# Performance work log

Measured on AMD Instinct MI355X. Metric: run time of the kernel, lower is better.

## Reference

```python
import jax, jax.numpy as jnp
import numpy as np

H = 8          # num_heads
SCALE = 25.0   # attention temperature
THRESH = 0.75  # raw cosine-similarity mask threshold


def _l2n(x):
    return x / jnp.linalg.norm(x, axis=-1, keepdims=True)


def setup_inputs() -> dict:
    key = jax.random.key(0)
    ks = jax.random.split(key, 8)
    B, N, C, OUT = 1, 2048, 1024, 1024
    s = 0.02
    return {
        "x_cls": jax.random.normal(ks[0], (B, N, C), jnp.float32),
        "x_reg": jax.random.normal(ks[1], (B, N, C), jnp.float32),
        "cls_score": jax.random.uniform(ks[2], (N,), jnp.float32),
        "fg_score": jax.random.uniform(ks[3], (N,), jnp.float32),
        "W_qkv_cls": jax.random.normal(ks[4], (3 * C, C), jnp.float32) * s,
        "W_qkv_reg": jax.random.normal(ks[5], (3 * C, C), jnp.float32) * s,
        "W1": jax.random.normal(ks[6], (2 * C, 2 * C), jnp.float32) * s,
        "b1": jnp.zeros((2 * C,), jnp.float32),
        "W2": jax.random.normal(ks[7], (OUT, 4 * C), jnp.float32) * s,
        "b2": jnp.zeros((OUT,), jnp.float32),
    }


def reference(x_cls, x_reg, cls_score, fg_score, W_qkv_cls, W_qkv_reg, W1, b1, W2, b2):
    B, N, C = x_cls.shape
    d = C // H

    def split_qkv(x, W):
        # nn.Linear (no bias): x @ W.T, then [B,N,3,H,d] -> [3,B,H,N,d]
        qkv = (x @ W.T).reshape(B, N, 3, H, d).transpose(2, 0, 3, 1, 4)
        return qkv[0], qkv[1], qkv[2]

    q_cls, k_cls, v_cls = split_qkv(x_cls, W_qkv_cls)
    q_reg, k_reg, _ = split_qkv(x_reg, W_qkv_reg)

    q_cls, k_cls = _l2n(q_cls), _l2n(k_cls)
    q_reg, k_reg = _l2n(q_reg), _l2n(k_reg)
    v_cls_n = _l2n(v_cls)

    cs = cls_score.reshape(1, 1, 1, N)  # broadcast over [B,H,N,N]
    fs = fg_score.reshape(1, 1, 1, N)

    attn_cls_raw = jnp.einsum('bhnd,bhmd->bhnm', v_cls_n, v_cls_n)
    attn_cls = jax.nn.softmax(jnp.einsum('bhnd,bhmd->bhnm', q_cls, k_cls) * SCALE * cs, axis=-1)
    attn_reg = jax.nn.softmax(jnp.einsum('bhnd,bhmd->bhnm', q_reg, k_reg) * SCALE * fs, axis=-1)
    attn = (attn_reg + attn_cls) * 0.5

    x = jnp.einsum('bhnm,bhmd->bhnd', attn, v_cls).transpose(0, 2, 1, 3).reshape(B, N, C)
    x_ori = v_cls.transpose(0, 2, 1, 3).reshape(B, N, C)
    trans_cls = jnp.concatenate([x, x_ori], axis=-1)  # [B,N,2C]

    # head-averaged similarity, masked and re-normalized (batch element 0)
    sim_raw = attn_cls_raw.sum(axis=1)[0] / H          # [N,N]
    sim_mask = (sim_raw > THRESH).astype(x_cls.dtype)
    sim_attn = attn.sum(axis=1)[0] / H
    sim_round2 = jax.nn.softmax(sim_attn, axis=-1)
    masked = sim_mask * sim_round2
    sim_round2 = masked / masked.sum(axis=-1, keepdims=True)

    msa = trans_cls @ W1.T + b1                        # linear1 [B,N,2C]
    feat = msa[0]                                      # [N,2C]
    soft_sim = sim_round2 @ feat                       # [N,2C]
    ave = jnp.concatenate([soft_sim, feat], axis=-1)   # [N,4C]
    out = ave @ W2.T + b2                              # [N,OUT]
    return out
```

## Files before the change

### kernel.cpp

```cpp
#include <hip/hip_runtime.h>
#include <math.h>

#define PN 2048
#define PC 1024
#define PH 8
#define PD 128
#define PC3 3072

typedef __bf16 bf16x8 __attribute__((ext_vector_type(8)));
typedef float  f32x4  __attribute__((ext_vector_type(4)));
typedef short  s8v    __attribute__((ext_vector_type(8)));
typedef short  s4v    __attribute__((ext_vector_type(4)));

__device__ __forceinline__ short f2bf(float x) {
    unsigned u = __float_as_uint(x);
    unsigned r = (u + 0x7fffu + ((u >> 16) & 1u)) >> 16;
    return (short)r;
}
__device__ __forceinline__ float bf2f(short s) {
    return __uint_as_float(((unsigned)(unsigned short)s) << 16);
}

#define LDS_DMA(g, l) __builtin_amdgcn_global_load_lds( \
    (const __attribute__((address_space(1))) void*)(g), \
    (__attribute__((address_space(3))) void*)(l), 16, 0, 0)

__device__ __forceinline__ void stage128(const short* g, long ld, short* lds,
                                         int wave, int lrow, int lcol)
{
#pragma unroll
    for (int kc = 0; kc < 4; ++kc) {
        LDS_DMA(g + (long)lrow * ld + kc * 32 + lcol, lds + kc * 4096 + wave * 512);
        LDS_DMA(g + (long)(lrow + 64) * ld + kc * 32 + lcol,
                lds + kc * 4096 + 2048 + wave * 512);
    }
}

template<int BN, bool OBF16, bool BIAS>
__global__ __launch_bounds__(256) void mfma_gemm_k(
    const short* __restrict__ A, int lda, long zsa,
    const short* __restrict__ B, int ldb, long zsb,
    void* __restrict__ Cv, int ldc, long zsc,
    int K, float alpha, const float* __restrict__ bias)
{
    constexpr int NJ = BN / 32;
    __shared__ short As[128 * 32];
    __shared__ short Bs[BN * 32];
    const int tid = threadIdx.x;
    const int wave = tid >> 6, lane = tid & 63;
    const int lrow = tid >> 2;
    const int lcol = (tid & 3) * 8;
    const int z = blockIdx.z;
    A += (long)z * zsa;
    B += (long)z * zsb;
    const int row0 = blockIdx.y * 128, col0 = blockIdx.x * BN;
    const short* Ag = A + (long)(row0 + lrow) * lda + lcol;
    const short* Bg = B + (long)(col0 + lrow) * ldb + lcol;
    short* AsW0 = As + wave * 512;
    short* AsW1 = As + 2048 + wave * 512;
    short* BsW0 = Bs + wave * 512;
    short* BsW1 = Bs + 2048 + wave * 512;
    const int wr = (wave >> 1) * 64, wc = (wave & 1) * (BN / 2);
    const int m16 = lane & 15, q8 = (lane >> 4) * 8;

    f32x4 acc[4][NJ];
#pragma unroll
    for (int i = 0; i < 4; ++i)
#pragma unroll
        for (int j = 0; j < NJ; ++j) acc[i][j] = (f32x4){0.f, 0.f, 0.f, 0.f};

    for (int kt = 0; kt < K; kt += 32) {
        if (kt) __syncthreads();
        LDS_DMA(Ag + kt, AsW0);
        LDS_DMA(Ag + kt + 64 * (long)lda, AsW1);
        LDS_DMA(Bg + kt, BsW0);
        if (BN == 128) LDS_DMA(Bg + kt + 64 * (long)ldb, BsW1);
        __syncthreads();
        bf16x8 a[4], b[NJ];
#pragma unroll
        for (int i = 0; i < 4; ++i)
            a[i] = *(const bf16x8*)&As[(wr + i * 16 + m16) * 32 + q8];
#pragma unroll
        for (int j = 0; j < NJ; ++j)
            b[j] = *(const bf16x8*)&Bs[(wc + j * 16 + m16) * 32 + q8];
#pragma unroll
        for (int i = 0; i < 4; ++i)
#pragma unroll
            for (int j = 0; j < NJ; ++j)
                acc[i][j] = __builtin_amdgcn_mfma_f32_16x16x32_bf16(a[i], b[j], acc[i][j], 0, 0, 0);
    }

    const long cz = (long)z * zsc;
#pragma unroll
    for (int i = 0; i < 4; ++i) {
        const int r0 = row0 + wr + i * 16 + (lane >> 4) * 4;
#pragma unroll
        for (int j = 0; j < NJ; ++j) {
            const int c = col0 + wc + j * 16 + m16;
            const float bv = BIAS ? bias[c] : 0.0f;
#pragma unroll
            for (int t = 0; t < 4; ++t) {
                const float x = acc[i][j][t] * alpha + bv;
                const long off = cz + (long)(r0 + t) * ldc + c;
                if (OBF16) ((short*)Cv)[off] = f2bf(x);
                else       ((float*)Cv)[off] = x;
            }
        }
    }
}

__global__ __launch_bounds__(256) void attn_rowsum_k(
    const short* __restrict__ qkv,
    const float* __restrict__ cls_score, const float* __restrict__ fg_score,
    float* __restrict__ l_g)
{
    __shared__ short Qs[16384];
    __shared__ short Ks[2][16384];
    __shared__ float lsum[128][2];
    const int tid = threadIdx.x, wave = tid >> 6, lane = tid & 63;
    const int lrow = tid >> 2, lcol = (tid & 3) * 8;
    const int wr = (wave >> 1) * 64, wc = (wave & 1) * 64;
    const int m16 = lane & 15, q4 = lane >> 4, q8 = q4 * 8;
    const int row0 = blockIdx.x * 128, h = blockIdx.y, side = blockIdx.z;
    const float* sc_g = side ? fg_score : cls_score;
    const short* base = qkv + (long)side * PN * PC3 + h * PD;
    const short* Kg = base + PC;
    stage128(base + (long)row0 * PC3, PC3, Qs, wave, lrow, lcol);
    stage128(Kg, PC3, Ks[0], wave, lrow, lcol);
    bf16x8 a[4][4];
    float rs[4][4] = {};
    for (int ct = 0; ct < 16; ++ct) {
        __syncthreads();
        if (ct == 0) {
#pragma unroll
            for (int i = 0; i < 4; ++i)
#pragma unroll
                for (int kc = 0; kc < 4; ++kc)
                    a[i][kc] = *(const bf16x8*)&Qs[kc * 4096 + (wr + i * 16 + m16) * 32 + q8];
        }
        if (ct < 15)
            stage128(Kg + (long)(ct + 1) * 128 * PC3, PC3, Ks[(ct + 1) & 1], wave, lrow, lcol);
        const short* kb = Ks[ct & 1];
        f32x4 acc[4][4];
#pragma unroll
        for (int i = 0; i < 4; ++i)
#pragma unroll
            for (int j = 0; j < 4; ++j) acc[i][j] = (f32x4){0.f, 0.f, 0.f, 0.f};
#pragma unroll
        for (int kc = 0; kc < 4; ++kc) {
            bf16x8 b[4];
#pragma unroll
            for (int j = 0; j < 4; ++j)
                b[j] = *(const bf16x8*)&kb[kc * 4096 + (wc + j * 16 + m16) * 32 + q8];
#pragma unroll
            for (int i = 0; i < 4; ++i)
#pragma unroll
                for (int j = 0; j < 4; ++j)
                    acc[i][j] = __builtin_amdgcn_mfma_f32_16x16x32_bf16(a[i][kc], b[j], acc[i][j], 0, 0, 0);
        }
#pragma unroll
        for (int j = 0; j < 4; ++j) {
            const float s25 = 25.0f * sc_g[ct * 128 + wc + j * 16 + m16];
#pragma unroll
            for (int i = 0; i < 4; ++i)
#pragma unroll
                for (int t = 0; t < 4; ++t)
                    rs[i][t] += __expf(acc[i][j][t] * s25);
        }
    }
#pragma unroll
    for (int i = 0; i < 4; ++i)
#pragma unroll
        for (int t = 0; t < 4; ++t) {
            float v = rs[i][t];
            v += __shfl_xor(v, 1, 64); v += __shfl_xor(v, 2, 64);
            v += __shfl_xor(v, 4, 64); v += __shfl_xor(v, 8, 64);
            if (m16 == 0) lsum[wr + i * 16 + q4 * 4 + t][wave & 1] = v;
        }
    __syncthreads();
    if (tid < 128)
        l_g[((long)side * PH + h) * PN + row0 + tid] = lsum[tid][0] + lsum[tid][1];
}

__global__ __launch_bounds__(256) void attn_combine_k(
    const short* __restrict__ qkv,
    const float* __restrict__ cls_score, const float* __restrict__ fg_score,
    const float* __restrict__ l_g,
    short* __restrict__ attn8, float* __restrict__ sim_attn)
{
    __shared__ short Ts[65536];
    const int tid = threadIdx.x, wave = tid >> 6, lane = tid & 63;
    const int lrow = tid >> 2, lcol = (tid & 3) * 8;
    const int wr = (wave >> 1) * 64, wc = (wave & 1) * 64;
    const int m16 = lane & 15, q4 = lane >> 4, q8 = q4 * 8;
    const int col0 = blockIdx.x * 128, row0 = blockIdx.y * 128;
    const long NN = (long)PN * PN;

    {
        const short* b0 = qkv;
        stage128(b0 + (long)row0 * PC3, PC3, Ts, wave, lrow, lcol);
        stage128(b0 + PC + (long)col0 * PC3, PC3, Ts + 16384, wave, lrow, lcol);
    }

    f32x4 sim[4][4];
#pragma unroll
    for (int i = 0; i < 4; ++i)
#pragma unroll
        for (int j = 0; j < 4; ++j) sim[i][j] = (f32x4){0.f, 0.f, 0.f, 0.f};
    f32x4 comb[4][4];

    for (int st = 0; st < 16; ++st) {
        const int h = st >> 1, s = st & 1;
        __syncthreads();
        if (st < 15) {
            const int h2 = (st + 1) >> 1, s2 = (st + 1) & 1;
            const short* b2 = qkv + (long)s2 * PN * PC3 + h2 * PD;
            short* dst = Ts + ((st + 1) & 1) * 32768;
            stage128(b2 + (long)row0 * PC3, PC3, dst, wave, lrow, lcol);
            stage128(b2 + PC + (long)col0 * PC3, PC3, dst + 16384, wave, lrow, lcol);
        }
        const short* Qb = Ts + (st & 1) * 32768;
        const short* Kb = Qb + 16384;

        float rl[4][4];
#pragma unroll
        for (int i = 0; i < 4; ++i)
#pragma unroll
            for (int t = 0; t < 4; ++t)
                rl[i][t] = 0.5f / l_g[((long)s * PH + h) * PN + row0 + wr + i * 16 + q4 * 4 + t];

        f32x4 acc[4][4];
#pragma unroll
        for (int i = 0; i < 4; ++i)
#pragma unroll
            for (int j = 0; j < 4; ++j) acc[i][j] = (f32x4){0.f, 0.f, 0.f, 0.f};
#pragma unroll
        for (int kc = 0; kc < 4; ++kc) {
            bf16x8 a[4], b[4];
#pragma unroll
            for (int i = 0; i < 4; ++i)
                a[i] = *(const bf16x8*)&Qb[kc * 4096 + (wr + i * 16 + m16) * 32 + q8];
#pragma unroll
            for (int j = 0; j < 4; ++j)
                b[j] = *(const bf16x8*)&Kb[kc * 4096 + (wc + j * 16 + m16) * 32 + q8];
#pragma unroll
            for (int i = 0; i < 4; ++i)
#pragma unroll
                for (int j = 0; j < 4; ++j)
                    acc[i][j] = __builtin_amdgcn_mfma_f32_16x16x32_bf16(a[i], b[j], acc[i][j], 0, 0, 0);
        }
        const float* sc_g = s ? fg_score : cls_score;
#pragma unroll
        for (int j = 0; j < 4; ++j) {
            const float s25 = 25.0f * sc_g[col0 + wc + j * 16 + m16];
#pragma unroll
            for (int i = 0; i < 4; ++i)
#pragma unroll
                for (int t = 0; t < 4; ++t) {
                    const float e = __expf(acc[i][j][t] * s25) * rl[i][t];
                    comb[i][j][t] = s ? (comb[i][j][t] + e) : e;
                }
        }
        if (s) {
#pragma unroll
            for (int i = 0; i < 4; ++i)
#pragma unroll
                for (int t = 0; t < 4; ++t) {
                    const long rbase = (long)h * NN +
                        (long)(row0 + wr + i * 16 + q4 * 4 + t) * PN + col0 + wc + m16;
#pragma unroll
                    for (int j = 0; j < 4; ++j)
                        attn8[rbase + j * 16] = f2bf(comb[i][j][t]);
                }
#pragma unroll
            for (int i = 0; i < 4; ++i)
#pragma unroll
                for (int j = 0; j < 4; ++j)
#pragma unroll
                    for (int t = 0; t < 4; ++t)
                        sim[i][j][t] += comb[i][j][t] * 0.125f;
        }
    }
#pragma unroll
    for (int i = 0; i < 4; ++i)
#pragma unroll
        for (int t = 0; t < 4; ++t) {
            const long rbase = (long)(row0 + wr + i * 16 + q4 * 4 + t) * PN + col0 + wc + m16;
#pragma unroll
            for (int j = 0; j < 4; ++j)
                sim_attn[rbase + j * 16] = sim[i][j][t];
        }
}

__global__ __launch_bounds__(256) void f2bf_k(const float* __restrict__ src,
                                              short* __restrict__ dst, int n4)
{
    const int i = blockIdx.x * 256 + threadIdx.x;
    if (i < n4) {
        float4 v = ((const float4*)src)[i];
        s4v o;
        o[0] = f2bf(v.x); o[1] = f2bf(v.y); o[2] = f2bf(v.z); o[3] = f2bf(v.w);
        ((s4v*)dst)[i] = o;
    }
}

__global__ __launch_bounds__(256) void transpose_bf16_k(
    const short* __restrict__ src, int sld, short* __restrict__ dst, int dld)
{
    __shared__ short tl[64][72];
    const int r0 = blockIdx.y * 64, c0 = blockIdx.x * 64;
    const int tr = threadIdx.x >> 2;
    const int tc = (threadIdx.x & 3) * 16;
    const short* sp = src + (long)(r0 + tr) * sld + c0 + tc;
    s8v v0 = *(const s8v*)sp;
    s8v v1 = *(const s8v*)(sp + 8);
    *(s8v*)&tl[tr][tc] = v0;
    *(s8v*)&tl[tr][tc + 8] = v1;
    __syncthreads();
    s8v o0, o1;
#pragma unroll
    for (int k = 0; k < 8; ++k) { o0[k] = tl[tc + k][tr]; o1[k] = tl[tc + 8 + k][tr]; }
    short* dp = dst + (long)(c0 + tr) * dld + r0 + tc;
    *(s8v*)dp = o0;
    *(s8v*)(dp + 8) = o1;
}

__global__ __launch_bounds__(256) void norm_qk_k(short* __restrict__ qkv)
{
    short* p = qkv + (long)blockIdx.z * ((long)PN * PC3)
                   + (long)blockIdx.x * PC3 + blockIdx.y * PC + threadIdx.x * 4;
    s4v v = *(s4v*)p;
    float f0 = bf2f(v[0]), f1 = bf2f(v[1]), f2 = bf2f(v[2]), f3 = bf2f(v[3]);
    float ss = f0 * f0 + f1 * f1 + f2 * f2 + f3 * f3;
    ss += __shfl_xor(ss, 16, 64); ss += __shfl_xor(ss, 8, 64);
    ss += __shfl_xor(ss, 4, 64);  ss += __shfl_xor(ss, 2, 64);
    ss += __shfl_xor(ss, 1, 64);
    const float rn = rsqrtf(ss);
    s4v o;
    o[0] = f2bf(f0 * rn); o[1] = f2bf(f1 * rn); o[2] = f2bf(f2 * rn); o[3] = f2bf(f3 * rn);
    *(s4v*)p = o;
}

__global__ __launch_bounds__(256) void norm_v_k(const short* __restrict__ qkv_cls,
                                                short* __restrict__ Vn,
                                                short* __restrict__ trans)
{
    const int n = blockIdx.x, t = threadIdx.x;
    const short* p = qkv_cls + (long)n * PC3 + 2 * PC + t * 4;
    s4v v = *(const s4v*)p;
    float f0 = bf2f(v[0]), f1 = bf2f(v[1]), f2 = bf2f(v[2]), f3 = bf2f(v[3]);
    float ss = f0 * f0 + f1 * f1 + f2 * f2 + f3 * f3;
    ss += __shfl_xor(ss, 16, 64); ss += __shfl_xor(ss, 8, 64);
    ss += __shfl_xor(ss, 4, 64);  ss += __shfl_xor(ss, 2, 64);
    ss += __shfl_xor(ss, 1, 64);
    const float rn = rsqrtf(ss);
    s4v o;
    o[0] = f2bf(f0 * rn); o[1] = f2bf(f1 * rn); o[2] = f2bf(f2 * rn); o[3] = f2bf(f3 * rn);
    *(s4v*)(Vn + (long)n * PC + t * 4) = o;
    *(s4v*)(trans + (long)n * (2 * PC) + PC + t * 4) = v;
}

__device__ __forceinline__ float wave_sum(float v) {
#pragma unroll
    for (int o = 32; o > 0; o >>= 1) v += __shfl_xor(v, o, 64);
    return v;
}
__device__ __forceinline__ float wave_max(float v) {
#pragma unroll
    for (int o = 32; o > 0; o >>= 1) v = fmaxf(v, __shfl_xor(v, o, 64));
    return v;
}
__device__ __forceinline__ float block_sum(float v, float* sm) {
    v = wave_sum(v);
    __syncthreads();
    if ((threadIdx.x & 63) == 0) sm[threadIdx.x >> 6] = v;
    __syncthreads();
    return sm[0] + sm[1] + sm[2] + sm[3];
}
__device__ __forceinline__ float block_max(float v, float* sm) {
    v = wave_max(v);
    __syncthreads();
    if ((threadIdx.x & 63) == 0) sm[threadIdx.x >> 6] = v;
    __syncthreads();
    return fmaxf(fmaxf(sm[0], sm[1]), fmaxf(sm[2], sm[3]));
}

__global__ __launch_bounds__(256) void sim_round2_k(
    const float* __restrict__ S, const short* __restrict__ Sraw,
    short* __restrict__ Sout)
{
    __shared__ float sm[4];
    const long row = (long)blockIdx.x * PN;
    const int t = threadIdx.x;
    float v[8];
    bool keep[8];
#pragma unroll
    for (int j = 0; j < 8; ++j) {
        const int m = t + 256 * j;
        v[j] = S[row + m];
        keep[j] = bf2f(Sraw[row + m]) > 0.75f;
    }
    float mx = -1e30f;
#pragma unroll
    for (int j = 0; j < 8; ++j) mx = fmaxf(mx, v[j]);
    mx = block_max(mx, sm);
    float sum = 0.f;
#pragma unroll
    for (int j = 0; j < 8; ++j) { v[j] = __expf(v[j] - mx); sum += v[j]; }
    sum = block_sum(sum, sm);
    const float inv = 1.0f / sum;
    float msum = 0.f;
#pragma unroll
    for (int j = 0; j < 8; ++j) { v[j] = keep[j] ? v[j] * inv : 0.f; msum += v[j]; }
    msum = block_sum(msum, sm);
    const float minv = 1.0f / msum;
#pragma unroll
    for (int j = 0; j < 8; ++j) {
        const int m = t + 256 * j;
        Sout[row + m] = f2bf(v[j] * minv);
    }
}

extern "C" void kernel_launch(void* const* d_in, const int* in_sizes, int n_in,
                              void* d_out, int out_size, void* d_ws, size_t ws_size,
                              hipStream_t stream)
{
    (void)in_sizes; (void)n_in; (void)out_size; (void)ws_size;
    const float* x_cls = (const float*)d_in[0];
    const float* x_reg = (const float*)d_in[1];
    const float* cls_score = (const float*)d_in[2];
    const float* fg_score = (const float*)d_in[3];
    const float* Wqc = (const float*)d_in[4];
    const float* Wqr = (const float*)d_in[5];
    const float* W1 = (const float*)d_in[6];
    const float* b1 = (const float*)d_in[7];
    const float* W2 = (const float*)d_in[8];
    const float* b2 = (const float*)d_in[9];
    float* out = (float*)d_out;

    char* w = (char*)d_ws;
    short* qkv_cls_bf = (short*)(w + ((size_t)0   << 20));
    short* qkv_reg_bf = (short*)(w + ((size_t)12  << 20));
    short* attn8      = (short*)(w + ((size_t)24  << 20));
    float* sim_attn   = (float*)(w + ((size_t)88  << 20));
    short* sim_raw_bf = (short*)(w + ((size_t)104 << 20));
    short* Vn         = (short*)(w + ((size_t)112 << 20));
    short* vT         = (short*)(w + ((size_t)116 << 20));
    short* W1_bf      = (short*)(w + ((size_t)120 << 20));
    short* W2_bf      = (short*)(w + ((size_t)128 << 20));
    short* x_cls_bf   = (short*)(w + ((size_t)136 << 20));
    short* x_reg_bf   = (short*)(w + ((size_t)140 << 20));
    short* Wqc_bf     = (short*)(w + ((size_t)144 << 20));
    short* Wqr_bf     = (short*)(w + ((size_t)150 << 20));
    float* l_g        = (float*)(w + ((size_t)160 << 20));
    short* trans      = (short*)(w + ((size_t)136 << 20));
    short* ave        = (short*)(w + ((size_t)144 << 20));
    short* sim_bf     = (short*)(w + ((size_t)24  << 20));
    short* featT      = (short*)(w + ((size_t)32  << 20));

    const long NN = (long)PN * PN;

    f2bf_k<<<2048, 256, 0, stream>>>(x_cls, x_cls_bf, PN * PC / 4);
    f2bf_k<<<2048, 256, 0, stream>>>(x_reg, x_reg_bf, PN * PC / 4);
    f2bf_k<<<3072, 256, 0, stream>>>(Wqc, Wqc_bf, PC3 * PC / 4);
    f2bf_k<<<3072, 256, 0, stream>>>(Wqr, Wqr_bf, PC3 * PC / 4);
    f2bf_k<<<4096, 256, 0, stream>>>(W1, W1_bf, 2 * PC * 2 * PC / 4);
    f2bf_k<<<4096, 256, 0, stream>>>(W2, W2_bf, PC * 4 * PC / 4);

    mfma_gemm_k<128, true, false><<<dim3(24, 16, 1), 256, 0, stream>>>(
        x_cls_bf, PC, 0, Wqc_bf, PC, 0, qkv_cls_bf, PC3, 0, PC, 1.0f, nullptr);
    mfma_gemm_k<128, true, false><<<dim3(16, 16, 1), 256, 0, stream>>>(
        x_reg_bf, PC, 0, Wqr_bf, PC, 0, qkv_reg_bf, PC3, 0, PC, 1.0f, nullptr);

    norm_qk_k<<<dim3(PN, 2, 2), 256, 0, stream>>>(qkv_cls_bf);
    norm_v_k<<<dim3(PN), 256, 0, stream>>>(qkv_cls_bf, Vn, trans);
    transpose_bf16_k<<<dim3(PC / 64, PN / 64), 256, 0, stream>>>(
        qkv_cls_bf + 2 * PC, PC3, vT, PN);

    mfma_gemm_k<128, true, false><<<dim3(16, 16, 1), 256, 0, stream>>>(
        Vn, PC, 0, Vn, PC, 0, sim_raw_bf, PN, 0, PC, 0.125f, nullptr);

    attn_rowsum_k<<<dim3(16, PH, 2), 256, 0, stream>>>(
        qkv_cls_bf, cls_score, fg_score, l_g);
    attn_combine_k<<<dim3(16, 16), 256, 0, stream>>>(
        qkv_cls_bf, cls_score, fg_score, l_g, attn8, sim_attn);

    mfma_gemm_k<64, true, false><<<dim3(2, 16, PH), 256, 0, stream>>>(
        attn8, PN, NN, vT, PN, (long)PD * PN, trans, 2 * PC, PD, PN, 1.0f, nullptr);

    sim_round2_k<<<PN, 256, 0, stream>>>(sim_attn, sim_raw_bf, sim_bf);

    mfma_gemm_k<128, true, true><<<dim3(16, 16, 1), 256, 0, stream>>>(
        trans, 2 * PC, 0, W1_bf, 2 * PC, 0, ave + 2 * PC, 4 * PC, 0, 2 * PC, 1.0f, b1);

    transpose_bf16_k<<<dim3(32, 32), 256, 0, stream>>>(ave + 2 * PC, 4 * PC, featT, 2 * PC);

    mfma_gemm_k<128, true, false><<<dim3(16, 16, 1), 256, 0, stream>>>(
        sim_bf, 2 * PC, 0, featT, 2 * PC, 0, ave, 4 * PC, 0, 2 * PC, 1.0f, nullptr);

    mfma_gemm_k<64, false, true><<<dim3(16, 16, 1), 256, 0, stream>>>(
        ave, 4 * PC, 0, W2_bf, 4 * PC, 0, out, PC, 0, 4 * PC, 1.0f, b2);
}
```

Measured before the change: 507.3 us.

## Single-buffer attention LDS, vectorize combine stores, merge conversion and norm launches

The attention rowsum and combine kernels drop LDS double buffering for a single buffer with extra barriers, halving shared memory per block so more blocks can be resident per CU. The combine kernel swaps the MFMA operand order so each lane holds contiguous columns, which lets it issue 4-wide vector stores for attn8 and sim_attn. The six fp32-to-bf16 conversion launches are merged into one kernel over a contiguous workspace, and the QK and V normalisation kernels are merged into one launch. The trade-off is that global loads no longer overlap with MFMA work inside a block, so the change relies on higher occupancy to hide that latency.

```diff
diff --git a/kernel.cpp b/kernel.cpp
--- a/kernel.cpp
+++ b/kernel.cpp
@@ -115,7 +115,7 @@
     float* __restrict__ l_g)
 {
     __shared__ short Qs[16384];
-    __shared__ short Ks[2][16384];
+    __shared__ short Ks[16384];
     __shared__ float lsum[128][2];
     const int tid = threadIdx.x, wave = tid >> 6, lane = tid & 63;
     const int lrow = tid >> 2, lcol = (tid & 3) * 8;
@@ -126,21 +126,21 @@
     const short* base = qkv + (long)side * PN * PC3 + h * PD;
     const short* Kg = base + PC;
     stage128(base + (long)row0 * PC3, PC3, Qs, wave, lrow, lcol);
-    stage128(Kg, PC3, Ks[0], wave, lrow, lcol);
+    stage128(Kg, PC3, Ks, wave, lrow, lcol);
+    __syncthreads();
     bf16x8 a[4][4];
+#pragma unroll
+    for (int i = 0; i < 4; ++i)
+#pragma unroll
+        for (int kc = 0; kc < 4; ++kc)
+            a[i][kc] = *(const bf16x8*)&Qs[kc * 4096 + (wr + i * 16 + m16) * 32 + q8];
     float rs[4][4] = {};
     for (int ct = 0; ct < 16; ++ct) {
-        __syncthreads();
-        if (ct == 0) {
-#pragma unroll
-            for (int i = 0; i < 4; ++i)
-#pragma unroll
-                for (int kc = 0; kc < 4; ++kc)
-                    a[i][kc] = *(const bf16x8*)&Qs[kc * 4096 + (wr + i * 16 + m16) * 32 + q8];
-        }
-        if (ct < 15)
-            stage128(Kg + (long)(ct + 1) * 128 * PC3, PC3, Ks[(ct + 1) & 1], wave, lrow, lcol);
-        const short* kb = Ks[ct & 1];
+        if (ct) {
+            __syncthreads();
+            stage128(Kg + (long)ct * 128 * PC3, PC3, Ks, wave, lrow, lcol);
+            __syncthreads();
+        }
         f32x4 acc[4][4];
 #pragma unroll
         for (int i = 0; i < 4; ++i)
@@ -151,7 +151,7 @@
             bf16x8 b[4];
 #pragma unroll
             for (int j = 0; j < 4; ++j)
-                b[j] = *(const bf16x8*)&kb[kc * 4096 + (wc + j * 16 + m16) * 32 + q8];
+                b[j] = *(const bf16x8*)&Ks[kc * 4096 + (wc + j * 16 + m16) * 32 + q8];
 #pragma unroll
             for (int i = 0; i < 4; ++i)
 #pragma unroll
@@ -188,7 +188,7 @@
     const float* __restrict__ l_g,
     short* __restrict__ attn8, float* __restrict__ sim_attn)
 {
-    __shared__ short Ts[65536];
+    __shared__ short Ts[32768];
     const int tid = threadIdx.x, wave = tid >> 6, lane = tid & 63;
     const int lrow = tid >> 2, lcol = (tid & 3) * 8;
     const int wr = (wave >> 1) * 64, wc = (wave & 1) * 64;
@@ -196,12 +196,6 @@
     const int col0 = blockIdx.x * 128, row0 = blockIdx.y * 128;
     const long NN = (long)PN * PN;
 
-    {
-        const short* b0 = qkv;
-        stage128(b0 + (long)row0 * PC3, PC3, Ts, wave, lrow, lcol);
-        stage128(b0 + PC + (long)col0 * PC3, PC3, Ts + 16384, wave, lrow, lcol);
-    }
-
     f32x4 sim[4][4];
 #pragma unroll
     for (int i = 0; i < 4; ++i)
@@ -211,97 +205,95 @@
 
     for (int st = 0; st < 16; ++st) {
         const int h = st >> 1, s = st & 1;
+        const short* bq = qkv + (long)s * PN * PC3 + h * PD;
         __syncthreads();
-        if (st < 15) {
-            const int h2 = (st + 1) >> 1, s2 = (st + 1) & 1;
-            const short* b2 = qkv + (long)s2 * PN * PC3 + h2 * PD;
-            short* dst = Ts + ((st + 1) & 1) * 32768;
-            stage128(b2 + (long)row0 * PC3, PC3, dst, wave, lrow, lcol);
-            stage128(b2 + PC + (long)col0 * PC3, PC3, dst + 16384, wave, lrow, lcol);
-        }
-        const short* Qb = Ts + (st & 1) * 32768;
-        const short* Kb = Qb + 16384;
-
-        float rl[4][4];
+        stage128(bq + (long)row0 * PC3, PC3, Ts, wave, lrow, lcol);
+        stage128(bq + PC + (long)col0 * PC3, PC3, Ts + 16384, wave, lrow, lcol);
+        __syncthreads();
+
+        float rl[4];
+#pragma unroll
+        for (int j = 0; j < 4; ++j)
+            rl[j] = 0.5f / l_g[((long)s * PH + h) * PN + row0 + wr + j * 16 + m16];
+
+        f32x4 acc[4][4];
 #pragma unroll
         for (int i = 0; i < 4; ++i)
 #pragma unroll
-            for (int t = 0; t < 4; ++t)
-                rl[i][t] = 0.5f / l_g[((long)s * PH + h) * PN + row0 + wr + i * 16 + q4 * 4 + t];
-
-        f32x4 acc[4][4];
-#pragma unroll
-        for (int i = 0; i < 4; ++i)
-#pragma unroll
             for (int j = 0; j < 4; ++j) acc[i][j] = (f32x4){0.f, 0.f, 0.f, 0.f};
 #pragma unroll
         for (int kc = 0; kc < 4; ++kc) {
-            bf16x8 a[4], b[4];
+            bf16x8 kf[4], qf[4];
 #pragma unroll
             for (int i = 0; i < 4; ++i)
-                a[i] = *(const bf16x8*)&Qb[kc * 4096 + (wr + i * 16 + m16) * 32 + q8];
+                kf[i] = *(const bf16x8*)&Ts[16384 + kc * 4096 + (wc + i * 16 + m16) * 32 + q8];
 #pragma unroll
             for (int j = 0; j < 4; ++j)
-                b[j] = *(const bf16x8*)&Kb[kc * 4096 + (wc + j * 16 + m16) * 32 + q8];
+                qf[j] = *(const bf16x8*)&Ts[kc * 4096 + (wr + j * 16 + m16) * 32 + q8];
 #pragma unroll
             for (int i = 0; i < 4; ++i)
 #pragma unroll
                 for (int j = 0; j < 4; ++j)
-                    acc[i][j] = __builtin_amdgcn_mfma_f32_16x16x32_bf16(a[i], b[j], acc[i][j], 0, 0, 0);
+                    acc[i][j] = __builtin_amdgcn_mfma_f32_16x16x32_bf16(kf[i], qf[j], acc[i][j], 0, 0, 0);
         }
         const float* sc_g = s ? fg_score : cls_score;
 #pragma unroll
-        for (int j = 0; j < 4; ++j) {
-            const float s25 = 25.0f * sc_g[col0 + wc + j * 16 + m16];
-#pragma unroll
-            for (int i = 0; i < 4; ++i)
+        for (int i = 0; i < 4; ++i) {
+            const f32x4 sc4 = *(const f32x4*)&sc_g[col0 + wc + i * 16 + q4 * 4];
+#pragma unroll
+            for (int j = 0; j < 4; ++j)
 #pragma unroll
                 for (int t = 0; t < 4; ++t) {
-                    const float e = __expf(acc[i][j][t] * s25) * rl[i][t];
+                    const float e = __expf(acc[i][j][t] * (25.0f * sc4[t])) * rl[j];
                     comb[i][j][t] = s ? (comb[i][j][t] + e) : e;
                 }
         }
         if (s) {
 #pragma unroll
-            for (int i = 0; i < 4; ++i)
-#pragma unroll
-                for (int t = 0; t < 4; ++t) {
-                    const long rbase = (long)h * NN +
-                        (long)(row0 + wr + i * 16 + q4 * 4 + t) * PN + col0 + wc + m16;
-#pragma unroll
-                    for (int j = 0; j < 4; ++j)
-                        attn8[rbase + j * 16] = f2bf(comb[i][j][t]);
+            for (int j = 0; j < 4; ++j) {
+                const long rb = (long)h * NN + (long)(row0 + wr + j * 16 + m16) * PN
+                              + col0 + wc + q4 * 4;
+#pragma unroll
+                for (int i = 0; i < 4; ++i) {
+                    s4v o;
+#pragma unroll
+                    for (int t = 0; t < 4; ++t) o[t] = f2bf(comb[i][j][t]);
+                    *(s4v*)&attn8[rb + i * 16] = o;
+                    sim[i][j] += comb[i][j] * 0.125f;
                 }
-#pragma unroll
-            for (int i = 0; i < 4; ++i)
-#pragma unroll
-                for (int j = 0; j < 4; ++j)
-#pragma unroll
-                    for (int t = 0; t < 4; ++t)
-                        sim[i][j][t] += comb[i][j][t] * 0.125f;
-        }
-    }
-#pragma unroll
-    for (int i = 0; i < 4; ++i)
-#pragma unroll
-        for (int t = 0; t < 4; ++t) {
-            const long rbase = (long)(row0 + wr + i * 16 + q4 * 4 + t) * PN + col0 + wc + m16;
-#pragma unroll
-            for (int j = 0; j < 4; ++j)
-                sim_attn[rbase + j * 16] = sim[i][j][t];
-        }
-}
-
-__global__ __launch_bounds__(256) void f2bf_k(const float* __restrict__ src,
-                                              short* __restrict__ dst, int n4)
-{
+            }
+        }
+    }
+#pragma unroll
+    for (int j = 0; j < 4; ++j) {
+        const long rb = (long)(row0 + wr + j * 16 + m16) * PN + col0 + wc + q4 * 4;
+#pragma unroll
+        for (int i = 0; i < 4; ++i)
+            *(f32x4*)&sim_attn[rb + i * 16] = sim[i][j];
+    }
+}
+
+__global__ __launch_bounds__(256) void f2bf6_k(
+    const float* __restrict__ s0, const float* __restrict__ s1,
+    const float* __restrict__ s2, const float* __restrict__ s3,
+    const float* __restrict__ s4, const float* __restrict__ s5,
+    short* __restrict__ dst)
+{
+    const int n0 = 512 * 1024, n1 = 512 * 1024, n2 = 768 * 1024,
+              n3 = 768 * 1024, n4 = 1024 * 1024;
     const int i = blockIdx.x * 256 + threadIdx.x;
-    if (i < n4) {
-        float4 v = ((const float4*)src)[i];
-        s4v o;
-        o[0] = f2bf(v.x); o[1] = f2bf(v.y); o[2] = f2bf(v.z); o[3] = f2bf(v.w);
-        ((s4v*)dst)[i] = o;
-    }
+    const float* src;
+    int j = i;
+    if (j < n0) src = s0;
+    else { j -= n0; if (j < n1) src = s1;
+    else { j -= n1; if (j < n2) src = s2;
+    else { j -= n2; if (j < n3) src = s3;
+    else { j -= n3; if (j < n4) src = s4;
+    else { j -= n4; src = s5; } } } } }
+    float4 v = ((const float4*)src)[j];
+    s4v o;
+    o[0] = f2bf(v.x); o[1] = f2bf(v.y); o[2] = f2bf(v.z); o[3] = f2bf(v.w);
+    ((s4v*)dst)[i] = o;
 }
 
 __global__ __launch_bounds__(256) void transpose_bf16_k(
@@ -325,39 +317,40 @@
     *(s8v*)(dp + 8) = o1;
 }
 
-__global__ __launch_bounds__(256) void norm_qk_k(short* __restrict__ qkv)
-{
-    short* p = qkv + (long)blockIdx.z * ((long)PN * PC3)
-                   + (long)blockIdx.x * PC3 + blockIdx.y * PC + threadIdx.x * 4;
-    s4v v = *(s4v*)p;
-    float f0 = bf2f(v[0]), f1 = bf2f(v[1]), f2 = bf2f(v[2]), f3 = bf2f(v[3]);
-    float ss = f0 * f0 + f1 * f1 + f2 * f2 + f3 * f3;
-    ss += __shfl_xor(ss, 16, 64); ss += __shfl_xor(ss, 8, 64);
-    ss += __shfl_xor(ss, 4, 64);  ss += __shfl_xor(ss, 2, 64);
-    ss += __shfl_xor(ss, 1, 64);
-    const float rn = rsqrtf(ss);
-    s4v o;
-    o[0] = f2bf(f0 * rn); o[1] = f2bf(f1 * rn); o[2] = f2bf(f2 * rn); o[3] = f2bf(f3 * rn);
-    *(s4v*)p = o;
-}
-
-__global__ __launch_bounds__(256) void norm_v_k(const short* __restrict__ qkv_cls,
-                                                short* __restrict__ Vn,
-                                                short* __restrict__ trans)
-{
-    const int n = blockIdx.x, t = threadIdx.x;
-    const short* p = qkv_cls + (long)n * PC3 + 2 * PC + t * 4;
-    s4v v = *(const s4v*)p;
-    float f0 = bf2f(v[0]), f1 = bf2f(v[1]), f2 = bf2f(v[2]), f3 = bf2f(v[3]);
-    float ss = f0 * f0 + f1 * f1 + f2 * f2 + f3 * f3;
-    ss += __shfl_xor(ss, 16, 64); ss += __shfl_xor(ss, 8, 64);
-    ss += __shfl_xor(ss, 4, 64);  ss += __shfl_xor(ss, 2, 64);
-    ss += __shfl_xor(ss, 1, 64);
-    const float rn = rsqrtf(ss);
-    s4v o;
-    o[0] = f2bf(f0 * rn); o[1] = f2bf(f1 * rn); o[2] = f2bf(f2 * rn); o[3] = f2bf(f3 * rn);
-    *(s4v*)(Vn + (long)n * PC + t * 4) = o;
-    *(s4v*)(trans + (long)n * (2 * PC) + PC + t * 4) = v;
+__global__ __launch_bounds__(256) void norms_k(short* __restrict__ qkv,
+                                               short* __restrict__ Vn,
+                                               short* __restrict__ trans)
+{
+    const int n = blockIdx.x, which = blockIdx.y, t = threadIdx.x;
+    if (which < 4) {
+        short* p = qkv + (long)(which >> 1) * ((long)PN * PC3)
+                 + (long)n * PC3 + (which & 1) * PC + t * 4;
+        s4v v = *(s4v*)p;
+        float f0 = bf2f(v[0]), f1 = bf2f(v[1]), f2 = bf2f(v[2]), f3 = bf2f(v[3]);
+        float ss = f0 * f0 + f1 * f1 + f2 * f2 + f3 * f3;
+        ss += __shfl_xor(ss, 16, 64); ss += __shfl_xor(ss, 8, 64);
+        ss += __shfl_xor(ss, 4, 64);  ss += __shfl_xor(ss, 2, 64);
+        ss += __shfl_xor(ss, 1, 64);
+        const float rn = rsqrtf(ss);
+        s4v o;
+        o[0] = f2bf(f0 * rn); o[1] = f2bf(f1 * rn);
+        o[2] = f2bf(f2 * rn); o[3] = f2bf(f3 * rn);
+        *(s4v*)p = o;
+    } else {
+        const short* p = qkv + (long)n * PC3 + 2 * PC + t * 4;
+        s4v v = *(const s4v*)p;
+        float f0 = bf2f(v[0]), f1 = bf2f(v[1]), f2 = bf2f(v[2]), f3 = bf2f(v[3]);
+        float ss = f0 * f0 + f1 * f1 + f2 * f2 + f3 * f3;
+        ss += __shfl_xor(ss, 16, 64); ss += __shfl_xor(ss, 8, 64);
+        ss += __shfl_xor(ss, 4, 64);  ss += __shfl_xor(ss, 2, 64);
+        ss += __shfl_xor(ss, 1, 64);
+        const float rn = rsqrtf(ss);
+        s4v o;
+        o[0] = f2bf(f0 * rn); o[1] = f2bf(f1 * rn);
+        o[2] = f2bf(f2 * rn); o[3] = f2bf(f3 * rn);
+        *(s4v*)(Vn + (long)n * PC + t * 4) = o;
+        *(s4v*)(trans + (long)n * (2 * PC) + PC + t * 4) = v;
+    }
 }
 
 __device__ __forceinline__ float wave_sum(float v) {
@@ -446,34 +439,29 @@
     short* sim_raw_bf = (short*)(w + ((size_t)104 << 20));
     short* Vn         = (short*)(w + ((size_t)112 << 20));
     short* vT         = (short*)(w + ((size_t)116 << 20));
-    short* W1_bf      = (short*)(w + ((size_t)120 << 20));
-    short* W2_bf      = (short*)(w + ((size_t)128 << 20));
-    short* x_cls_bf   = (short*)(w + ((size_t)136 << 20));
-    short* x_reg_bf   = (short*)(w + ((size_t)140 << 20));
-    short* Wqc_bf     = (short*)(w + ((size_t)144 << 20));
-    short* Wqr_bf     = (short*)(w + ((size_t)150 << 20));
-    float* l_g        = (float*)(w + ((size_t)160 << 20));
-    short* trans      = (short*)(w + ((size_t)136 << 20));
-    short* ave        = (short*)(w + ((size_t)144 << 20));
+    short* bf_all     = (short*)(w + ((size_t)120 << 20));
+    short* x_cls_bf   = bf_all;
+    short* x_reg_bf   = (short*)(w + ((size_t)124 << 20));
+    short* Wqc_bf     = (short*)(w + ((size_t)128 << 20));
+    short* Wqr_bf     = (short*)(w + ((size_t)134 << 20));
+    short* W1_bf      = (short*)(w + ((size_t)140 << 20));
+    short* W2_bf      = (short*)(w + ((size_t)148 << 20));
+    float* l_g        = (float*)(w + ((size_t)156 << 20));
+    short* trans      = (short*)(w + ((size_t)120 << 20));
     short* sim_bf     = (short*)(w + ((size_t)24  << 20));
     short* featT      = (short*)(w + ((size_t)32  << 20));
+    short* ave        = (short*)(w + ((size_t)40  << 20));
 
     const long NN = (long)PN * PN;
 
-    f2bf_k<<<2048, 256, 0, stream>>>(x_cls, x_cls_bf, PN * PC / 4);
-    f2bf_k<<<2048, 256, 0, stream>>>(x_reg, x_reg_bf, PN * PC / 4);
-    f2bf_k<<<3072, 256, 0, stream>>>(Wqc, Wqc_bf, PC3 * PC / 4);
-    f2bf_k<<<3072, 256, 0, stream>>>(Wqr, Wqr_bf, PC3 * PC / 4);
-    f2bf_k<<<4096, 256, 0, stream>>>(W1, W1_bf, 2 * PC * 2 * PC / 4);
-    f2bf_k<<<4096, 256, 0, stream>>>(W2, W2_bf, PC * 4 * PC / 4);
+    f2bf6_k<<<18432, 256, 0, stream>>>(x_cls, x_reg, Wqc, Wqr, W1, W2, bf_all);
 
     mfma_gemm_k<128, true, false><<<dim3(24, 16, 1), 256, 0, stream>>>(
         x_cls_bf, PC, 0, Wqc_bf, PC, 0, qkv_cls_bf, PC3, 0, PC, 1.0f, nullptr);
     mfma_gemm_k<128, true, false><<<dim3(16, 16, 1), 256, 0, stream>>>(
         x_reg_bf, PC, 0, Wqr_bf, PC, 0, qkv_reg_bf, PC3, 0, PC, 1.0f, nullptr);
 
-    norm_qk_k<<<dim3(PN, 2, 2), 256, 0, stream>>>(qkv_cls_bf);
-    norm_v_k<<<dim3(PN), 256, 0, stream>>>(qkv_cls_bf, Vn, trans);
+    norms_k<<<dim3(PN, 5), 256, 0, stream>>>(qkv_cls_bf, Vn, trans);
     transpose_bf16_k<<<dim3(PC / 64, PN / 64), 256, 0, stream>>>(
         qkv_cls_bf + 2 * PC, PC3, vT, PN);
 
```

Result: no change. 504.1 us (-0.6%).
